# Performance work log

Measured on AMD Instinct MI355X. Metric: run time of the kernel, lower is better.

The kernel has to match this reference:

```python
import jax, jax.numpy as jnp
import numpy as np

B = 64          # num_graphs per batch
ADJ = 1000      # adj_shape (nodes per graph)
N = B * ADJ     # total nodes
E = 1 << 20     # edges
M = 32000       # selected (batch, node) pairs
D_IN = 128
D_OUT = 128


def setup_inputs() -> dict:
    key = jax.random.key(0)
    ks = jax.random.split(key, 12)
    inp = {
        "x0": jax.random.normal(ks[0], (N, D_IN), jnp.float32),
        "x1": jax.random.normal(ks[1], (N, D_IN), jnp.float32),
        "edge_index": jax.random.randint(ks[2], (2, E), 0, N, jnp.int64),
        "b_idx0": jax.random.randint(ks[3], (M,), 0, B, jnp.int64),
        "n_idx0": jax.random.randint(ks[4], (M,), 0, ADJ, jnp.int64),
        "b_idx1": jax.random.randint(ks[5], (M,), 0, B, jnp.int64),
        "n_idx1": jax.random.randint(ks[6], (M,), 0, ADJ, jnp.int64),
        "W1": jax.random.normal(ks[7], (D_IN, D_IN), jnp.float32) / np.sqrt(D_IN),
        "b1": jnp.zeros((D_IN,), jnp.float32),
        "W2": jax.random.normal(ks[8], (D_IN, D_IN), jnp.float32) / np.sqrt(D_IN),
        "b2": jnp.zeros((D_IN,), jnp.float32),
        "Wl": jax.random.normal(ks[9], (D_IN, D_OUT), jnp.float32) / np.sqrt(D_IN),
        "bl": jnp.zeros((D_OUT,), jnp.float32),
        "Wfi": jax.random.normal(ks[10], (D_IN, D_OUT), jnp.float32) / np.sqrt(D_IN),
        "bfi": jnp.zeros((D_OUT,), jnp.float32),
    }
    return inp


def _gnn_layer(h, edge_index, W, b):
    # GCN-style message passing: gather source features, scatter-sum to dst,
    # then linear project.  h: [N, d]
    msgs = h[edge_index[0]]                                    # [E, d] gather
    agg = jax.ops.segment_sum(msgs, edge_index[1], num_segments=N)  # [N, d]
    return agg @ W + b


def reference(x0, x1, edge_index, b_idx0, n_idx0, b_idx1, n_idx1,
              W1, b1, W2, b2, Wl, bl, Wfi, bfi):
    # branch i == 0: raw features -> 2D gather -> fc_in
    d0 = x0.reshape(B, ADJ, -1)[b_idx0, n_idx0]                # [M, D_IN]
    d0 = d0 @ Wfi + bfi                                        # [M, D_OUT]

    # branch i == 1 (observ=True): gnn1 -> gnn2 -> 2D gather -> linear
    # (dropout omitted for deterministic reference; p=0.2 at train time)
    h = _gnn_layer(x1, edge_index, W1, b1)
    h = _gnn_layer(h, edge_index, W2, b2)
    d1 = h.reshape(B, ADJ, -1)[b_idx1, n_idx1]                 # [M, D_IN]
    d1 = d1 @ Wl + bl                                          # [M, D_OUT]

    return jnp.stack([d0, d1])                                 # [2, M, D_OUT]
```

## Files before the change

kernel.cpp:

```cpp
#include <hip/hip_runtime.h>
#include <hip/hip_bf16.h>


#define B_    64
#define ADJ_  1000
#define N_    64000
#define E_    (1 << 20)
#define M_    32000
#define DV    128
#define CAP   64
#define RANGES 8
#define RSPAN  (N_ / RANGES)
#define CHUNKS 512
#define EPB    (E_ / CHUNKS)

typedef __attribute__((ext_vector_type(8))) short short8v;
typedef __attribute__((ext_vector_type(4))) float float4v;

__device__ __forceinline__ float u2f(unsigned int u) {
  union { unsigned int i; float f; } x; x.i = u; return x.f;
}
__device__ __forceinline__ unsigned short f2bf(float f) {
  union { float f; unsigned int i; } x; x.f = f;
  unsigned int r = x.i + 0x7fffu + ((x.i >> 16) & 1u);
  return (unsigned short)(r >> 16);
}
__device__ __forceinline__ unsigned int pack_bf2(float a, float b) {
  __hip_bfloat162 h = __float22bfloat162_rn(float2{a, b});
  union { __hip_bfloat162 h; unsigned int u; } c; c.h = h;
  return c.u;
}

__device__ __forceinline__ void fill_part(const int* __restrict__ ei,
                                          int* __restrict__ counts,
                                          unsigned short* __restrict__ bucket,
                                          int c, int r) {
  const int* srcA = ei;
  const int* dstA = ei + E_;
  int lo = r * RSPAN;
  int t4 = c * EPB + (int)threadIdx.x * 4;
  int4 d0 = *(const int4*)(dstA + t4);
  int4 s0 = *(const int4*)(srcA + t4);
  int4 d1 = *(const int4*)(dstA + t4 + 1024);
  int4 s1 = *(const int4*)(srcA + t4 + 1024);
#define PROC(D, S) do {                                                \
    if ((unsigned)((D) - lo) < (unsigned)RSPAN) {                      \
      int pos = atomicAdd(&counts[(D)], 1);                            \
      if (pos < CAP) bucket[(D) * CAP + pos] = (unsigned short)(S);    \
    } } while (0)
  PROC(d0.x, s0.x); PROC(d0.y, s0.y); PROC(d0.z, s0.z); PROC(d0.w, s0.w);
  PROC(d1.x, s1.x); PROC(d1.y, s1.y); PROC(d1.z, s1.z); PROC(d1.w, s1.w);
#undef PROC
}

template<bool GATHER, bool ABF16, bool OUTBF16, bool HASBIAS>
__device__ __forceinline__ void gemm_tile(const void* __restrict__ in,
                                          const float* __restrict__ W,
                                          const float* __restrict__ bias,
                                          void* __restrict__ out_, int tile,
                                          const int* __restrict__ bidx,
                                          const int* __restrict__ nidx,
                                          unsigned short* __restrict__ Bs) {
  int tid = threadIdx.x;
#pragma unroll 8
  for (int i = 0; i < 64; i++) {
    int g = i * 256 + tid;
    int k = g >> 7, n = g & 127;
    int addr = ((((n >> 4) * 4 + (k >> 5)) * 64 + ((k >> 3) & 3) * 16 + (n & 15)) << 3)
             + (k & 7);
    Bs[addr] = f2bf(W[g]);
  }
  __syncthreads();

  int lane = tid & 63;
  int wv   = tid >> 6;
  int m    = lane & 15;
  int q    = lane >> 4;
  int rbase = tile * 64 + wv * 16;
  int r     = rbase + m;

  size_t ir;
  if (GATHER) ir = (size_t)bidx[r] * ADJ_ + nidx[r];
  else        ir = (size_t)r;

  short8v af[4];
  if (ABF16) {
    const unsigned short* arow = (const unsigned short*)in + ir * DV;
#pragma unroll
    for (int kc = 0; kc < 4; kc++)
      af[kc] = *(const short8v*)(arow + kc * 32 + q * 8);
  } else {
    const float* arow = (const float*)in + ir * DV;
#pragma unroll
    for (int kc = 0; kc < 4; kc++) {
      const float4* p = (const float4*)(arow + kc * 32 + q * 8);
      float4 f0 = p[0], f1 = p[1];
      union { short8v s; unsigned int u[4]; } t;
      t.u[0] = pack_bf2(f0.x, f0.y);
      t.u[1] = pack_bf2(f0.z, f0.w);
      t.u[2] = pack_bf2(f1.x, f1.y);
      t.u[3] = pack_bf2(f1.z, f1.w);
      af[kc] = t.s;
    }
  }

  float4v acc[8];
#pragma unroll
  for (int nb = 0; nb < 8; nb++) acc[nb] = (float4v){0.f, 0.f, 0.f, 0.f};
#pragma unroll
  for (int nb = 0; nb < 8; nb++)
#pragma unroll
    for (int kc = 0; kc < 4; kc++) {
      short8v bf = *(const short8v*)(Bs + (((nb * 4 + kc) * 64 + lane) << 3));
      acc[nb] = __builtin_amdgcn_mfma_f32_16x16x32_bf16(af[kc], bf, acc[nb], 0, 0, 0);
    }

#pragma unroll
  for (int nb = 0; nb < 8; nb++) {
    float bvn = HASBIAS ? bias[nb * 16 + m] : 0.f;
    int col = nb * 16 + m;
#pragma unroll
    for (int i = 0; i < 4; i++) {
      int row = rbase + q * 4 + i;
      float v = acc[nb][i] + bvn;
      if (OUTBF16) ((unsigned short*)out_)[(size_t)row * DV + col] = f2bf(v);
      else         ((float*)out_)[(size_t)row * DV + col] = v;
    }
  }
}

__global__ __launch_bounds__(256)
void k1_fused(const int* __restrict__ ei, int* __restrict__ counts,
              unsigned short* __restrict__ bucket,
              const float* __restrict__ x1, const float* __restrict__ W1,
              unsigned int* __restrict__ t_bf,
              const float* __restrict__ x0, const float* __restrict__ Wfi,
              const float* __restrict__ bfi, float* __restrict__ out0,
              const int* __restrict__ b0, const int* __restrict__ n0i) {
  __shared__ unsigned short Bs[16384];
  int g = blockIdx.x >> 4, rem = blockIdx.x & 15;
  if (rem < 8) { fill_part(ei, counts, bucket, g, rem); return; }
  int o = g * 8 + rem - 8;
  if (o < 1000)
    gemm_tile<false, false, true, false>(x1, W1, nullptr, t_bf, o, nullptr, nullptr, Bs);
  else if (o < 1500)
    gemm_tile<true, false, false, true>(x0, Wfi, bfi, out0, o - 1000, b0, n0i, Bs);
}

template<bool GATHER, bool ABF16, bool OUTBF16, bool HASBIAS>
__global__ __launch_bounds__(256)
void gemm_k(const void* __restrict__ in, const float* __restrict__ W,
            const float* __restrict__ bias, void* __restrict__ out_,
            const int* __restrict__ bidx, const int* __restrict__ nidx) {
  __shared__ unsigned short Bs[16384];
  gemm_tile<GATHER, ABF16, OUTBF16, HASBIAS>(in, W, bias, out_, blockIdx.x, bidx, nidx, Bs);
}

template<bool OUTBF16, bool SEL>
__global__ __launch_bounds__(256)
void aggregate_k(const unsigned int* __restrict__ x,
                 const int* __restrict__ counts,
                 const unsigned short* __restrict__ bucket,
                 const float* __restrict__ bias, void* __restrict__ out_,
                 const int* __restrict__ bidx, const int* __restrict__ nidx) {
  int w    = (blockIdx.x * 256 + threadIdx.x) >> 6;
  int lane = threadIdx.x & 63;
  int node = SEL ? (bidx[w] * ADJ_ + nidx[w]) : w;
  int cnt = counts[node]; cnt = min(cnt, CAP);
  int mysrc = (int)bucket[node * CAP + lane];
  float2 bv = ((const float2*)bias)[lane];
  float2 acc; acc.x = bv.x; acc.y = bv.y;

  int d = 0;
  for (; d + 4 <= cnt; d += 4) {
    int s0 = __shfl(mysrc, d, 64);
    int s1 = __shfl(mysrc, d + 1, 64);
    int s2 = __shfl(mysrc, d + 2, 64);
    int s3 = __shfl(mysrc, d + 3, 64);
    unsigned int u0 = x[(size_t)s0 * 64 + lane];
    unsigned int u1 = x[(size_t)s1 * 64 + lane];
    unsigned int u2 = x[(size_t)s2 * 64 + lane];
    unsigned int u3 = x[(size_t)s3 * 64 + lane];
    acc.x += (u2f(u0 << 16) + u2f(u1 << 16)) + (u2f(u2 << 16) + u2f(u3 << 16));
    acc.y += (u2f(u0 & 0xffff0000u) + u2f(u1 & 0xffff0000u))
           + (u2f(u2 & 0xffff0000u) + u2f(u3 & 0xffff0000u));
  }
  for (; d < cnt; d++) {
    int s = __shfl(mysrc, d, 64);
    unsigned int u = x[(size_t)s * 64 + lane];
    acc.x += u2f(u << 16);
    acc.y += u2f(u & 0xffff0000u);
  }
  if (OUTBF16) ((unsigned int*)out_)[(size_t)w * 64 + lane] = pack_bf2(acc.x, acc.y);
  else         ((float2*)out_)[(size_t)w * 64 + lane] = acc;
}

extern "C" void kernel_launch(void* const* d_in, const int* in_sizes, int n_in,
                              void* d_out, int out_size, void* d_ws, size_t ws_size,
                              hipStream_t stream) {
  const float* x0  = (const float*)d_in[0];
  const float* x1  = (const float*)d_in[1];
  const int*   ei  = (const int*)  d_in[2];
  const int*   b0  = (const int*)  d_in[3];
  const int*   n0i = (const int*)  d_in[4];
  const int*   b1  = (const int*)  d_in[5];
  const int*   n1i = (const int*)  d_in[6];
  const float* W1  = (const float*)d_in[7];
  const float* bb1 = (const float*)d_in[8];
  const float* W2  = (const float*)d_in[9];
  const float* bb2 = (const float*)d_in[10];
  const float* Wl  = (const float*)d_in[11];
  const float* bl  = (const float*)d_in[12];
  const float* Wfi = (const float*)d_in[13];
  const float* bfi = (const float*)d_in[14];
  float* out = (float*)d_out;

  unsigned int*   t_bf   = (unsigned int*)d_ws;
  unsigned int*   h_bf   = t_bf + (size_t)N_ * 64;
  unsigned int*   sel_bf = h_bf + (size_t)N_ * 64;
  int*            counts = (int*)(sel_bf + (size_t)M_ * 64);
  unsigned short* bucket = (unsigned short*)(counts + N_);

  hipMemsetAsync(counts, 0, N_ * sizeof(int), stream);

  k1_fused<<<512 * 16, 256, 0, stream>>>(ei, counts, bucket, x1, W1, t_bf,
                                         x0, Wfi, bfi, out, b0, n0i);

  aggregate_k<true, false><<<N_ / 4, 256, 0, stream>>>(t_bf, counts, bucket, bb1,
                                                       h_bf, nullptr, nullptr);
  gemm_k<false, true, true, false><<<N_ / 64, 256, 0, stream>>>(h_bf, W2, nullptr,
                                                                t_bf, nullptr, nullptr);
  aggregate_k<true, true><<<M_ / 4, 256, 0, stream>>>(t_bf, counts, bucket, bb2,
                                                      sel_bf, b1, n1i);
  gemm_k<false, true, false, true><<<M_ / 64, 256, 0, stream>>>(sel_bf, Wl, bl,
                                                                out + (size_t)M_ * DV,
                                                                nullptr, nullptr);
}
```

Baseline: 266.9 us.

## Pre-convert weights to bf16 swizzled layout once and halve GEMM LDS footprint

```diff
diff --git a/kernel.cpp b/kernel.cpp
--- a/kernel.cpp
+++ b/kernel.cpp
@@ -29,6 +29,29 @@
   __hip_bfloat162 h = __float22bfloat162_rn(float2{a, b});
   union { __hip_bfloat162 h; unsigned int u; } c; c.h = h;
   return c.u;
+}
+
+__global__ __launch_bounds__(256)
+void prep_k(const float* __restrict__ W1, const float* __restrict__ Wfi,
+            const float* __restrict__ W2, const float* __restrict__ Wl,
+            unsigned short* __restrict__ Wbf, int* __restrict__ counts) {
+  int b = blockIdx.x, t = threadIdx.x;
+  int mi = b >> 3;
+  const float* W = (mi == 0) ? W1 : (mi == 1) ? Wfi : (mi == 2) ? W2 : Wl;
+  unsigned short* out = Wbf + mi * 16384;
+  int base = (b & 7) * 2048 + t * 8;
+  float4 f0 = *(const float4*)(W + base);
+  float4 f1 = *(const float4*)(W + base + 4);
+  float v[8] = {f0.x, f0.y, f0.z, f0.w, f1.x, f1.y, f1.z, f1.w};
+#pragma unroll
+  for (int u = 0; u < 8; u++) {
+    int g = base + u;
+    int k = g >> 7, n = g & 127;
+    int addr = ((((n >> 4) * 4 + (k >> 5)) * 64 + ((k >> 3) & 3) * 16 + (n & 15)) << 3)
+             + (k & 7);
+    out[addr] = f2bf(v[u]);
+  }
+  for (int i = b * 256 + t; i < N_; i += 32 * 256) counts[i] = 0;
 }
 
 __device__ __forceinline__ void fill_part(const int* __restrict__ ei,
@@ -55,29 +78,26 @@
 
 template<bool GATHER, bool ABF16, bool OUTBF16, bool HASBIAS>
 __device__ __forceinline__ void gemm_tile(const void* __restrict__ in,
-                                          const float* __restrict__ W,
+                                          const unsigned short* __restrict__ Wbf,
                                           const float* __restrict__ bias,
                                           void* __restrict__ out_, int tile,
                                           const int* __restrict__ bidx,
                                           const int* __restrict__ nidx,
                                           unsigned short* __restrict__ Bs) {
-  int tid = threadIdx.x;
-#pragma unroll 8
-  for (int i = 0; i < 64; i++) {
-    int g = i * 256 + tid;
-    int k = g >> 7, n = g & 127;
-    int addr = ((((n >> 4) * 4 + (k >> 5)) * 64 + ((k >> 3) & 3) * 16 + (n & 15)) << 3)
-             + (k & 7);
-    Bs[addr] = f2bf(W[g]);
-  }
-  __syncthreads();
-
+  int tid  = threadIdx.x;
   int lane = tid & 63;
   int wv   = tid >> 6;
   int m    = lane & 15;
   int q    = lane >> 4;
   int rbase = tile * 64 + wv * 16;
   int r     = rbase + m;
+
+  const short8v* Wv  = (const short8v*)Wbf;
+  short8v*       Bsv = (short8v*)Bs;
+
+  short8v w[4];
+#pragma unroll
+  for (int i = 0; i < 4; i++) w[i] = Wv[tid + i * 256];
 
   size_t ir;
   if (GATHER) ir = (size_t)bidx[r] * ADJ_ + nidx[r];
@@ -104,14 +124,33 @@
     }
   }
 
+#pragma unroll
+  for (int i = 0; i < 4; i++) Bsv[tid + i * 256] = w[i];
+  __syncthreads();
+
   float4v acc[8];
 #pragma unroll
   for (int nb = 0; nb < 8; nb++) acc[nb] = (float4v){0.f, 0.f, 0.f, 0.f};
-#pragma unroll
-  for (int nb = 0; nb < 8; nb++)
+
+#pragma unroll
+  for (int i = 0; i < 4; i++) w[i] = Wv[1024 + tid + i * 256];
+
+#pragma unroll
+  for (int nb = 0; nb < 4; nb++)
 #pragma unroll
     for (int kc = 0; kc < 4; kc++) {
-      short8v bf = *(const short8v*)(Bs + (((nb * 4 + kc) * 64 + lane) << 3));
+      short8v bf = Bsv[(nb * 4 + kc) * 64 + lane];
+      acc[nb] = __builtin_amdgcn_mfma_f32_16x16x32_bf16(af[kc], bf, acc[nb], 0, 0, 0);
+    }
+  __syncthreads();
+#pragma unroll
+  for (int i = 0; i < 4; i++) Bsv[tid + i * 256] = w[i];
+  __syncthreads();
+#pragma unroll
+  for (int nb = 4; nb < 8; nb++)
+#pragma unroll
+    for (int kc = 0; kc < 4; kc++) {
+      short8v bf = Bsv[((nb - 4) * 4 + kc) * 64 + lane];
       acc[nb] = __builtin_amdgcn_mfma_f32_16x16x32_bf16(af[kc], bf, acc[nb], 0, 0, 0);
     }
 
@@ -132,28 +171,28 @@
 __global__ __launch_bounds__(256)
 void k1_fused(const int* __restrict__ ei, int* __restrict__ counts,
               unsigned short* __restrict__ bucket,
-              const float* __restrict__ x1, const float* __restrict__ W1,
+              const float* __restrict__ x1, const unsigned short* __restrict__ Wbf,
               unsigned int* __restrict__ t_bf,
-              const float* __restrict__ x0, const float* __restrict__ Wfi,
-              const float* __restrict__ bfi, float* __restrict__ out0,
+              const float* __restrict__ x0, const float* __restrict__ bfi,
+              float* __restrict__ out0,
               const int* __restrict__ b0, const int* __restrict__ n0i) {
-  __shared__ unsigned short Bs[16384];
+  __shared__ unsigned short Bs[8192];
   int g = blockIdx.x >> 4, rem = blockIdx.x & 15;
   if (rem < 8) { fill_part(ei, counts, bucket, g, rem); return; }
   int o = g * 8 + rem - 8;
   if (o < 1000)
-    gemm_tile<false, false, true, false>(x1, W1, nullptr, t_bf, o, nullptr, nullptr, Bs);
+    gemm_tile<false, false, true, false>(x1, Wbf, nullptr, t_bf, o, nullptr, nullptr, Bs);
   else if (o < 1500)
-    gemm_tile<true, false, false, true>(x0, Wfi, bfi, out0, o - 1000, b0, n0i, Bs);
+    gemm_tile<true, false, false, true>(x0, Wbf + 16384, bfi, out0, o - 1000, b0, n0i, Bs);
 }
 
 template<bool GATHER, bool ABF16, bool OUTBF16, bool HASBIAS>
 __global__ __launch_bounds__(256)
-void gemm_k(const void* __restrict__ in, const float* __restrict__ W,
+void gemm_k(const void* __restrict__ in, const unsigned short* __restrict__ Wbf,
             const float* __restrict__ bias, void* __restrict__ out_,
             const int* __restrict__ bidx, const int* __restrict__ nidx) {
-  __shared__ unsigned short Bs[16384];
-  gemm_tile<GATHER, ABF16, OUTBF16, HASBIAS>(in, W, bias, out_, blockIdx.x, bidx, nidx, Bs);
+  __shared__ unsigned short Bs[8192];
+  gemm_tile<GATHER, ABF16, OUTBF16, HASBIAS>(in, Wbf, bias, out_, blockIdx.x, bidx, nidx, Bs);
 }
 
 template<bool OUTBF16, bool SEL>
@@ -172,8 +211,32 @@
   float2 acc; acc.x = bv.x; acc.y = bv.y;
 
   int d = 0;
-  for (; d + 4 <= cnt; d += 4) {
-    int s0 = __shfl(mysrc, d, 64);
+  for (; d + 8 <= cnt; d += 8) {
+    int s0 = __shfl(mysrc, d,     64);
+    int s1 = __shfl(mysrc, d + 1, 64);
+    int s2 = __shfl(mysrc, d + 2, 64);
+    int s3 = __shfl(mysrc, d + 3, 64);
+    int s4 = __shfl(mysrc, d + 4, 64);
+    int s5 = __shfl(mysrc, d + 5, 64);
+    int s6 = __shfl(mysrc, d + 6, 64);
+    int s7 = __shfl(mysrc, d + 7, 64);
+    unsigned int u0 = x[(size_t)s0 * 64 + lane];
+    unsigned int u1 = x[(size_t)s1 * 64 + lane];
+    unsigned int u2 = x[(size_t)s2 * 64 + lane];
+    unsigned int u3 = x[(size_t)s3 * 64 + lane];
+    unsigned int u4 = x[(size_t)s4 * 64 + lane];
+    unsigned int u5 = x[(size_t)s5 * 64 + lane];
+    unsigned int u6 = x[(size_t)s6 * 64 + lane];
+    unsigned int u7 = x[(size_t)s7 * 64 + lane];
+    acc.x += ((u2f(u0 << 16) + u2f(u1 << 16)) + (u2f(u2 << 16) + u2f(u3 << 16)))
+           + ((u2f(u4 << 16) + u2f(u5 << 16)) + (u2f(u6 << 16) + u2f(u7 << 16)));
+    acc.y += ((u2f(u0 & 0xffff0000u) + u2f(u1 & 0xffff0000u))
+            + (u2f(u2 & 0xffff0000u) + u2f(u3 & 0xffff0000u)))
+           + ((u2f(u4 & 0xffff0000u) + u2f(u5 & 0xffff0000u))
+            + (u2f(u6 & 0xffff0000u) + u2f(u7 & 0xffff0000u)));
+  }
+  if (d + 4 <= cnt) {
+    int s0 = __shfl(mysrc, d,     64);
     int s1 = __shfl(mysrc, d + 1, 64);
     int s2 = __shfl(mysrc, d + 2, 64);
     int s3 = __shfl(mysrc, d + 3, 64);
@@ -184,6 +247,7 @@
     acc.x += (u2f(u0 << 16) + u2f(u1 << 16)) + (u2f(u2 << 16) + u2f(u3 << 16));
     acc.y += (u2f(u0 & 0xffff0000u) + u2f(u1 & 0xffff0000u))
            + (u2f(u2 & 0xffff0000u) + u2f(u3 & 0xffff0000u));
+    d += 4;
   }
   for (; d < cnt; d++) {
     int s = __shfl(mysrc, d, 64);
@@ -220,19 +284,21 @@
   unsigned int*   sel_bf = h_bf + (size_t)N_ * 64;
   int*            counts = (int*)(sel_bf + (size_t)M_ * 64);
   unsigned short* bucket = (unsigned short*)(counts + N_);
-
-  hipMemsetAsync(counts, 0, N_ * sizeof(int), stream);
-
-  k1_fused<<<512 * 16, 256, 0, stream>>>(ei, counts, bucket, x1, W1, t_bf,
-                                         x0, Wfi, bfi, out, b0, n0i);
+  unsigned short* Wbf    = bucket + (size_t)N_ * CAP;
+
+  prep_k<<<32, 256, 0, stream>>>(W1, Wfi, W2, Wl, Wbf, counts);
+
+  k1_fused<<<512 * 16, 256, 0, stream>>>(ei, counts, bucket, x1, Wbf, t_bf,
+                                         x0, bfi, out, b0, n0i);
 
   aggregate_k<true, false><<<N_ / 4, 256, 0, stream>>>(t_bf, counts, bucket, bb1,
                                                        h_bf, nullptr, nullptr);
-  gemm_k<false, true, true, false><<<N_ / 64, 256, 0, stream>>>(h_bf, W2, nullptr,
-                                                                t_bf, nullptr, nullptr);
+  gemm_k<false, true, true, false><<<N_ / 64, 256, 0, stream>>>(h_bf, Wbf + 2 * 16384,
+                                                                nullptr, t_bf,
+                                                                nullptr, nullptr);
   aggregate_k<true, true><<<M_ / 4, 256, 0, stream>>>(t_bf, counts, bucket, bb2,
                                                       sel_bf, b1, n1i);
-  gemm_k<false, true, false, true><<<M_ / 64, 256, 0, stream>>>(sel_bf, Wl, bl,
-                                                                out + (size_t)M_ * DV,
+  gemm_k<false, true, false, true><<<M_ / 64, 256, 0, stream>>>(sel_bf, Wbf + 3 * 16384,
+                                                                bl, out + (size_t)M_ * DV,
                                                                 nullptr, nullptr);
 }
```

After: 262.5 us. Within noise of the previous version (-1.7%).
